# Kernel tuning notes

Hardware: AMD Instinct MI355X
Metric: run time of the kernel (lower is better)

Reference implementation:

```python
import jax, jax.numpy as jnp
import numpy as np

N, E, L, G, D = 131072, 262144, 16384, 2048, 300
NUM_LAYERS = 5


def setup_inputs() -> dict:
    key = jax.random.key(0)
    ks = jax.random.split(key, 16)
    s = 0.05
    inp = {}
    inp["x"] = jax.random.randint(ks[0], (N, 2), 0, 3, dtype=jnp.int32)
    inp["edge_index"] = jax.random.randint(ks[1], (2, E), 0, N, dtype=jnp.int32)
    inp["edge_attr"] = jax.random.randint(ks[2], (E, 2), 0, 3, dtype=jnp.int32)
    inp["lower_batch"] = jnp.sort(jax.random.randint(ks[3], (N,), 0, L, dtype=jnp.int32))
    inp["upper_batch"] = jnp.sort(jax.random.randint(ks[4], (L,), 0, G, dtype=jnp.int32))
    inp["x_emb1"] = jax.random.normal(ks[5], (120, D), jnp.float32) * s
    inp["x_emb2"] = jax.random.normal(ks[6], (3, D), jnp.float32) * s
    inp["edge_emb1"] = jax.random.normal(ks[7], (NUM_LAYERS, 6, D), jnp.float32) * s
    inp["edge_emb2"] = jax.random.normal(ks[8], (NUM_LAYERS, 3, D), jnp.float32) * s
    inp["mlp_w1"] = jax.random.normal(ks[9], (NUM_LAYERS, D, 2 * D), jnp.float32) * s
    inp["mlp_b1"] = jnp.zeros((NUM_LAYERS, 2 * D), jnp.float32)
    inp["mlp_w2"] = jax.random.normal(ks[10], (NUM_LAYERS, 2 * D, D), jnp.float32) * s
    inp["mlp_b2"] = jnp.zeros((NUM_LAYERS, D), jnp.float32)
    inp["bn_gamma"] = jnp.ones((NUM_LAYERS, D), jnp.float32)
    inp["bn_beta"] = jnp.zeros((NUM_LAYERS, D), jnp.float32)
    inp["cls_w1"] = jax.random.normal(ks[11], (D, D), jnp.float32) * s
    inp["cls_b1"] = jnp.zeros((D,), jnp.float32)
    inp["cls_w2"] = jax.random.normal(ks[12], (D, 1), jnp.float32) * s
    inp["cls_b2"] = jnp.zeros((1,), jnp.float32)
    return inp


def _segment_mean(data, seg, num):
    s = jax.ops.segment_sum(data, seg, num_segments=num)
    c = jax.ops.segment_sum(jnp.ones((data.shape[0], 1), data.dtype), seg, num_segments=num)
    return s / jnp.maximum(c, 1.0)


def reference(x, edge_index, edge_attr, lower_batch, upper_batch,
              x_emb1, x_emb2, edge_emb1, edge_emb2,
              mlp_w1, mlp_b1, mlp_w2, mlp_b2, bn_gamma, bn_beta,
              cls_w1, cls_b1, cls_w2, cls_b2):
    eps = 1e-5
    # node embeddings
    h = x_emb1[x[:, 0]] + x_emb2[x[:, 1]]  # [N, D]
    # add self loops with edge_attr (4, 0)
    loop = jnp.arange(N, dtype=edge_index.dtype)
    src = jnp.concatenate([edge_index[0], loop])
    dst = jnp.concatenate([edge_index[1], loop])
    ea0 = jnp.concatenate([edge_attr[:, 0], jnp.full((N,), 4, edge_attr.dtype)])
    ea1 = jnp.concatenate([edge_attr[:, 1], jnp.zeros((N,), edge_attr.dtype)])
    for l in range(NUM_LAYERS):
        e = edge_emb1[l][ea0] + edge_emb2[l][ea1]        # [E+N, D]
        msg = h[src] + e                                  # gather + add
        agg = jax.ops.segment_sum(msg, dst, num_segments=N)  # scatter-add
        h2 = jax.nn.relu(agg @ mlp_w1[l] + mlp_b1[l]) @ mlp_w2[l] + mlp_b2[l]
        # BatchNorm1d (training mode, biased var)
        mu = jnp.mean(h2, axis=0)
        var = jnp.var(h2, axis=0)
        h2 = (h2 - mu) * jax.lax.rsqrt(var + eps) * bn_gamma[l] + bn_beta[l]
        h = h2 if l == NUM_LAYERS - 1 else jax.nn.relu(h2)
    # hierarchical pooling: node -> lower substructure (mean), lower -> graph (mean)
    lower = _segment_mean(h, lower_batch, L)  # [L, D]

    def classify(feat):
        pooled = _segment_mean(feat, upper_batch, G)  # [G, D]
        hh = jax.nn.relu(pooled @ cls_w1 + cls_b1)
        return (hh @ cls_w2 + cls_b2)[:, 0]

    logits0 = classify(lower)
    logits1 = classify(jnp.roll(lower, 1, axis=0))  # aug_type == 'roll'
    return jnp.concatenate([logits0, logits1])  # [2G]
```

## Files before the change

kernel.cpp:

```cpp
#include <hip/hip_runtime.h>

#define N_NODES 131072
#define E_EDGES 262144
#define L_SEG 16384
#define G_SEG 2048
#define D_FEAT 300
#define NUM_LAYERS 5
#define MCHUNK 65536
#define HS 304
#define KP1 320
#define KP2 608
#define NP1 640
#define NP2 384

typedef unsigned short u16;
typedef unsigned int u32;
typedef __attribute__((ext_vector_type(8))) short short8v;
typedef __attribute__((ext_vector_type(4))) float f32x4;

struct __align__(16) U128 { u32 a, b, c, d; };
struct __align__(8) U64 { u32 a, b; };

__device__ __forceinline__ float bf2f(u16 u) { return __uint_as_float(((u32)u) << 16); }
__device__ __forceinline__ u16 f2bf(float f) {
  u32 x = __float_as_uint(f);
  x += 0x7fffu + ((x >> 16) & 1u);
  return (u16)(x >> 16);
}
__device__ __forceinline__ u32 pack2(float x, float y) {
  return (u32)f2bf(x) | ((u32)f2bf(y) << 16);
}

__device__ __forceinline__ void gl2lds16(const void* g, void* l) {
  auto gp = reinterpret_cast<const __attribute__((address_space(1))) void*>(
      reinterpret_cast<uintptr_t>(g));
  auto lp = reinterpret_cast<__attribute__((address_space(3))) void*>(
      reinterpret_cast<uintptr_t>(l));
  __builtin_amdgcn_global_load_lds(gp, lp, 16, 0, 0);
}

__global__ void k_init_h(const int* __restrict__ x, const float* __restrict__ e1,
                         const float* __restrict__ e2, u16* __restrict__ h) {
  int i = blockIdx.x * blockDim.x + threadIdx.x;
  if (i >= N_NODES * 76) return;
  int n = i / 76, q = i - n * 76;
  int col = q * 4;
  ushort4 o = make_ushort4(0, 0, 0, 0);
  if (col < 300) {
    int x0 = x[2 * n], x1 = x[2 * n + 1];
    float4 va = *(const float4*)(e1 + (size_t)x0 * D_FEAT + col);
    float4 vb = *(const float4*)(e2 + (size_t)x1 * D_FEAT + col);
    o.x = f2bf(va.x + vb.x); o.y = f2bf(va.y + vb.y);
    o.z = f2bf(va.z + vb.z); o.w = f2bf(va.w + vb.w);
  }
  *(ushort4*)(h + (size_t)n * HS + col) = o;
}

__global__ void k_prepw(const float* __restrict__ w, u16* __restrict__ wt,
                        int K, int Ncol, int NP, int KP) {
  int l = blockIdx.y;
  int i = blockIdx.x * blockDim.x + threadIdx.x;
  if (i >= NP * KP) return;
  int n = i / KP, k = i - n * KP;
  float v = (n < Ncol && k < K) ? w[(size_t)l * K * Ncol + (size_t)k * Ncol + n] : 0.f;
  wt[(size_t)l * NP * KP + i] = f2bf(v);
}

__global__ void k_zero(float* __restrict__ p, int n) {
  int i = blockIdx.x * blockDim.x + threadIdx.x;
  if (i < n) p[i] = 0.f;
}
__global__ void k_hist(const int* __restrict__ ei, int* __restrict__ cnt) {
  int e = blockIdx.x * blockDim.x + threadIdx.x;
  if (e < E_EDGES) atomicAdd(&cnt[ei[E_EDGES + e]], 1);
}
__global__ __launch_bounds__(1024) void k_scan(const int* __restrict__ cnt,
                                               int* __restrict__ offs,
                                               int* __restrict__ cursor) {
  __shared__ int part[1024];
  int t = threadIdx.x;
  int base = t * 128;
  int s = 0;
  for (int i = 0; i < 128; i++) s += cnt[base + i];
  part[t] = s;
  __syncthreads();
  for (int off = 1; off < 1024; off <<= 1) {
    int v = (t >= off) ? part[t - off] : 0;
    __syncthreads();
    part[t] += v;
    __syncthreads();
  }
  int run = (t == 0) ? 0 : part[t - 1];
  for (int i = 0; i < 128; i++) {
    offs[base + i] = run;
    cursor[base + i] = run;
    run += cnt[base + i];
  }
  if (t == 1023) offs[N_NODES] = run;
}
__global__ void k_fill(const int* __restrict__ ei, int* __restrict__ cursor,
                       int* __restrict__ elist) {
  int e = blockIdx.x * blockDim.x + threadIdx.x;
  if (e < E_EDGES) {
    int p = atomicAdd(&cursor[ei[E_EDGES + e]], 1);
    elist[p] = e;
  }
}

__global__ void k_gather(const u32* __restrict__ h, const int* __restrict__ ei,
                         const int* __restrict__ ea, const int* __restrict__ offs,
                         const int* __restrict__ elist, const float* __restrict__ sc1,
                         const float* __restrict__ sc2, const float* __restrict__ ee1,
                         const float* __restrict__ ee2, u32* __restrict__ agg) {
  int n = (blockIdx.x << 2) + (threadIdx.x >> 6);
  int lane = threadIdx.x & 63;
  int j0 = lane, j1 = lane + 64, j2 = lane + 128;
  float ax0, ay0, ax1, ay1, ax2 = 0.f, ay2 = 0.f;
  const u32* hn = h + (size_t)n * (HS / 2);
  {
    u32 u = hn[j0];
    ax0 = bf2f((u16)(u & 0xffffu)) + sc1[2 * j0] + sc2[2 * j0];
    ay0 = bf2f((u16)(u >> 16)) + sc1[2 * j0 + 1] + sc2[2 * j0 + 1];
    u = hn[j1];
    ax1 = bf2f((u16)(u & 0xffffu)) + sc1[2 * j1] + sc2[2 * j1];
    ay1 = bf2f((u16)(u >> 16)) + sc1[2 * j1 + 1] + sc2[2 * j1 + 1];
    if (j2 < 150) {
      u = hn[j2];
      ax2 = bf2f((u16)(u & 0xffffu)) + sc1[2 * j2] + sc2[2 * j2];
      ay2 = bf2f((u16)(u >> 16)) + sc1[2 * j2 + 1] + sc2[2 * j2 + 1];
    }
  }
  int p = offs[n], pe = offs[n + 1];
  int e, s, a0, a1;
  if (p < pe) {
    e = elist[p];
    s = ei[e];
    a0 = ea[2 * e];
    a1 = ea[2 * e + 1];
  }
  while (p < pe) {
    int np = p + 1;
    int e2 = 0, s2 = 0, a02 = 0, a12 = 0;
    if (np < pe) {
      e2 = elist[np];
      s2 = ei[e2];
      a02 = ea[2 * e2];
      a12 = ea[2 * e2 + 1];
    }
    const u32* hs = h + (size_t)s * (HS / 2);
    const float* p1 = ee1 + (size_t)a0 * D_FEAT;
    const float* p2 = ee2 + (size_t)a1 * D_FEAT;
    u32 u = hs[j0];
    ax0 += bf2f((u16)(u & 0xffffu)) + p1[2 * j0] + p2[2 * j0];
    ay0 += bf2f((u16)(u >> 16)) + p1[2 * j0 + 1] + p2[2 * j0 + 1];
    u = hs[j1];
    ax1 += bf2f((u16)(u & 0xffffu)) + p1[2 * j1] + p2[2 * j1];
    ay1 += bf2f((u16)(u >> 16)) + p1[2 * j1 + 1] + p2[2 * j1 + 1];
    if (j2 < 150) {
      u = hs[j2];
      ax2 += bf2f((u16)(u & 0xffffu)) + p1[2 * j2] + p2[2 * j2];
      ay2 += bf2f((u16)(u >> 16)) + p1[2 * j2 + 1] + p2[2 * j2 + 1];
    }
    p = np; e = e2; s = s2; a0 = a02; a1 = a12;
  }
  u32* ao = agg + (size_t)n * (KP1 / 2);
  ao[j0] = pack2(ax0, ay0);
  ao[j1] = pack2(ax1, ay1);
  if (j2 < 150) ao[j2] = pack2(ax2, ay2);
  else if (j2 < 160) ao[j2] = 0u;
}

template <bool RELU, int KP>
__global__ __launch_bounds__(512) void k_gemm_mfma(const u16* __restrict__ A,
                                                   const u16* __restrict__ WT,
                                                   const float* __restrict__ bias,
                                                   u16* __restrict__ C, int Ncol,
                                                   int Cstride, float* __restrict__ stats) {
  __shared__ __align__(16) u16 SL[12288];
  u16* Al = SL;
  u16* Bl = SL + 8192;
  int t = threadIdx.x;
  int w = t >> 6, lane = t & 63;
  int brow = blockIdx.y << 8, bcol = blockIdx.x << 7;
  int wr = w >> 1, wc = w & 1;
  int r16 = lane & 15, kq = lane >> 4;
  int rq = kq << 2;

  f32x4 zero4 = {0.f, 0.f, 0.f, 0.f};
  f32x4 acc[4][4];
#pragma unroll
  for (int mi = 0; mi < 4; mi++)
#pragma unroll
    for (int nj = 0; nj < 4; nj++) acc[mi][nj] = zero4;

  int m0 = 2 * w, m1 = m0 + 1;
  const u16* gA0 = A + (size_t)(brow + m0 * 16 + r16) * KP + kq * 8;
  const u16* gA1 = A + (size_t)(brow + m1 * 16 + r16) * KP + kq * 8;
  const u16* gB = WT + (size_t)(bcol + w * 16 + r16) * KP + kq * 8;
  u16* lA0 = Al + m0 * 512;
  u16* lA1 = Al + m1 * 512;
  u16* lB = Bl + w * 512;

  for (int k0 = 0; k0 < KP; k0 += 32) {
    __syncthreads();
    gl2lds16(gA0 + k0, lA0);
    gl2lds16(gA1 + k0, lA1);
    gl2lds16(gB + k0, lB);
    __syncthreads();
    short8v af[4], bf[4];
#pragma unroll
    for (int mi = 0; mi < 4; mi++)
      af[mi] = *(const short8v*)(Al + (wr * 4 + mi) * 512 + lane * 8);
#pragma unroll
    for (int nj = 0; nj < 4; nj++)
      bf[nj] = *(const short8v*)(Bl + (wc * 4 + nj) * 512 + lane * 8);
#pragma unroll
    for (int mi = 0; mi < 4; mi++)
#pragma unroll
      for (int nj = 0; nj < 4; nj++)
        acc[mi][nj] = __builtin_amdgcn_mfma_f32_16x16x32_bf16(af[mi], bf[nj], acc[mi][nj], 0, 0, 0);
  }

  __syncthreads();
#pragma unroll
  for (int p = 0; p < 4; p++) {
    if (wr == p) {
#pragma unroll
      for (int nj = 0; nj < 4; nj++) {
        int col = wc * 64 + nj * 16 + r16;
        int gcol = bcol + col;
        bool live = gcol < Ncol;
        float bs = live ? bias[gcol] : 0.f;
#pragma unroll
        for (int mi = 0; mi < 4; mi++) {
#pragma unroll
          for (int j = 0; j < 4; j++) {
            float v = acc[mi][nj][j] + bs;
            if (RELU) v = fmaxf(v, 0.f);
            if (!live) v = 0.f;
            SL[(mi * 16 + rq + j) * 132 + col] = f2bf(v);
          }
        }
      }
    }
    __syncthreads();
    {
      int r = t >> 3, s = t & 7;
      size_t grow = (size_t)(brow + p * 64 + r) * Cstride;
#pragma unroll
      for (int c = 0; c < 2; c++) {
        int colu = s * 16 + c * 8;
        int gcol = bcol + colu;
        if (gcol + 8 <= Cstride) {
          U64 v0 = *(const U64*)(SL + r * 132 + colu);
          U64 v1 = *(const U64*)(SL + r * 132 + colu + 4);
          *(U64*)(C + grow + gcol) = v0;
          *(U64*)(C + grow + gcol + 4) = v1;
        }
      }
    }
    if (stats != nullptr && t < 128) {
      int gcol = bcol + t;
      if (gcol < Ncol) {
        float s0 = 0.f, q0 = 0.f;
#pragma unroll 8
        for (int r = 0; r < 64; r++) {
          float v = bf2f(SL[r * 132 + t]);
          s0 += v;
          q0 = fmaf(v, v, q0);
        }
        atomicAdd(stats + gcol, s0);
        atomicAdd(stats + 304 + gcol, q0);
      }
    }
    __syncthreads();
  }
}

__global__ void k_bnfin(const float* __restrict__ sums, const float* __restrict__ gamma,
                        const float* __restrict__ beta, float* __restrict__ fa,
                        float* __restrict__ fc) {
  int d = blockIdx.x * blockDim.x + threadIdx.x;
  if (d >= HS) return;
  float a = 0.f, c = 0.f;
  if (d < D_FEAT) {
    const float inv = 1.f / (float)N_NODES;
    float mu = sums[d] * inv;
    float var = sums[304 + d] * inv - mu * mu;
    a = rsqrtf(var + 1e-5f) * gamma[d];
    c = beta[d] - mu * a;
  }
  fa[d] = a;
  fc[d] = c;
}

__global__ void k_bnnorm(u16* __restrict__ h, const float* __restrict__ fa,
                         const float* __restrict__ fc, int relu) {
  int i = blockIdx.x * blockDim.x + threadIdx.x;
  if (i >= N_NODES * 38) return;
  int n = i / 38, q = i - n * 38;
  int col = q * 8;
  u16* hp = h + (size_t)n * HS + col;
  float4 a0 = *(const float4*)(fa + col);
  float4 a1 = *(const float4*)(fa + col + 4);
  float4 c0 = *(const float4*)(fc + col);
  float4 c1 = *(const float4*)(fc + col + 4);
  ushort4 u0 = *(ushort4*)hp;
  ushort4 u1 = *(ushort4*)(hp + 4);
  float r0, r1, r2, r3, r4, r5, r6, r7;
#define BN1(res, uv, A, C)                       \
  res = fmaf((A), bf2f(uv), (C));                \
  if (relu) res = fmaxf(res, 0.f);
  BN1(r0, u0.x, a0.x, c0.x) BN1(r1, u0.y, a0.y, c0.y)
  BN1(r2, u0.z, a0.z, c0.z) BN1(r3, u0.w, a0.w, c0.w)
  BN1(r4, u1.x, a1.x, c1.x) BN1(r5, u1.y, a1.y, c1.y)
  BN1(r6, u1.z, a1.z, c1.z) BN1(r7, u1.w, a1.w, c1.w)
#undef BN1
  ushort4 o0, o1;
  o0.x = f2bf(r0); o0.y = f2bf(r1); o0.z = f2bf(r2); o0.w = f2bf(r3);
  o1.x = f2bf(r4); o1.y = f2bf(r5); o1.z = f2bf(r6); o1.w = f2bf(r7);
  *(ushort4*)hp = o0;
  *(ushort4*)(hp + 4) = o1;
}

__device__ __forceinline__ int lowerBound(const int* __restrict__ a, int n, int v) {
  int lo = 0, hi = n;
  while (lo < hi) {
    int m = (lo + hi) >> 1;
    if (a[m] < v) lo = m + 1; else hi = m;
  }
  return lo;
}

__global__ void k_lower(const u16* __restrict__ h, const int* __restrict__ lb,
                        float* __restrict__ lower) {
  int g = blockIdx.x;
  int s = lowerBound(lb, N_NODES, g);
  int e = lowerBound(lb, N_NODES, g + 1);
  float invc = 1.f / (float)max(e - s, 1);
  for (int d = threadIdx.x; d < D_FEAT; d += 256) {
    float acc = 0.f;
    for (int r = s; r < e; r++) acc += bf2f(h[(size_t)r * HS + d]);
    lower[(size_t)g * D_FEAT + d] = acc * invc;
  }
}

__global__ void k_pooled(const float* __restrict__ lower, const int* __restrict__ ub,
                         float* __restrict__ pooled) {
  int g = blockIdx.x, br = blockIdx.y;
  int s = lowerBound(ub, L_SEG, g);
  int e = lowerBound(ub, L_SEG, g + 1);
  float invc = 1.f / (float)max(e - s, 1);
  for (int d = threadIdx.x; d < D_FEAT; d += 256) {
    float acc = 0.f;
    for (int i = s; i < e; i++) {
      int row = br ? (i - 1 + L_SEG) % L_SEG : i;
      acc += lower[(size_t)row * D_FEAT + d];
    }
    pooled[((size_t)br * G_SEG + g) * D_FEAT + d] = acc * invc;
  }
}

__global__ __launch_bounds__(256) void k_classify(const float* __restrict__ pooled,
                                                  const float* __restrict__ w1,
                                                  const float* __restrict__ b1,
                                                  const float* __restrict__ w2,
                                                  const float* __restrict__ b2,
                                                  float* __restrict__ out) {
  __shared__ float p[D_FEAT];
  __shared__ float red[4];
  int g = blockIdx.x, br = blockIdx.y;
  const float* pr = pooled + ((size_t)br * G_SEG + g) * D_FEAT;
  for (int d = threadIdx.x; d < D_FEAT; d += 256) p[d] = pr[d];
  __syncthreads();
  float partial = 0.f;
  for (int j = threadIdx.x; j < D_FEAT; j += 256) {
    float acc = b1[j];
    for (int k = 0; k < D_FEAT; k++) acc = fmaf(p[k], w1[(size_t)k * D_FEAT + j], acc);
    acc = fmaxf(acc, 0.f);
    partial += acc * w2[j];
  }
  for (int off = 32; off; off >>= 1) partial += __shfl_down(partial, off, 64);
  int lane = threadIdx.x & 63, wid = threadIdx.x >> 6;
  if (lane == 0) red[wid] = partial;
  __syncthreads();
  if (threadIdx.x == 0) out[(size_t)br * G_SEG + g] = red[0] + red[1] + red[2] + red[3] + b2[0];
}

extern "C" void kernel_launch(void* const* d_in, const int* in_sizes, int n_in,
                              void* d_out, int out_size, void* d_ws, size_t ws_size,
                              hipStream_t stream) {
  const int* x = (const int*)d_in[0];
  const int* ei = (const int*)d_in[1];
  const int* ea = (const int*)d_in[2];
  const int* lb = (const int*)d_in[3];
  const int* ub = (const int*)d_in[4];
  const float* xe1 = (const float*)d_in[5];
  const float* xe2 = (const float*)d_in[6];
  const float* ee1 = (const float*)d_in[7];
  const float* ee2 = (const float*)d_in[8];
  const float* w1 = (const float*)d_in[9];
  const float* b1 = (const float*)d_in[10];
  const float* w2 = (const float*)d_in[11];
  const float* b2 = (const float*)d_in[12];
  const float* gam = (const float*)d_in[13];
  const float* bet = (const float*)d_in[14];
  const float* cw1 = (const float*)d_in[15];
  const float* cb1 = (const float*)d_in[16];
  const float* cw2 = (const float*)d_in[17];
  const float* cb2 = (const float*)d_in[18];
  float* out = (float*)d_out;

  char* base = (char*)d_ws;
  size_t off = 0;
  auto alloc = [&](size_t bytes) -> void* {
    void* p = base + off;
    off += (bytes + 255) & ~(size_t)255;
    return p;
  };
  u16* h = (u16*)alloc((size_t)N_NODES * HS * 2);
  u16* agg = (u16*)alloc((size_t)N_NODES * KP1 * 2);
  u16* tbuf = (u16*)alloc((size_t)MCHUNK * KP2 * 2);
  u16* W1T = (u16*)alloc((size_t)NUM_LAYERS * NP1 * KP1 * 2);
  u16* W2T = (u16*)alloc((size_t)NUM_LAYERS * NP2 * KP2 * 2);
  int* cnt = (int*)alloc((size_t)N_NODES * 4);
  int* offs = (int*)alloc((size_t)(N_NODES + 1) * 4);
  int* cursor = (int*)alloc((size_t)N_NODES * 4);
  int* elist = (int*)alloc((size_t)E_EDGES * 4);
  float* stats = (float*)alloc(608 * 4);
  float* aff_a = (float*)alloc(HS * 4);
  float* aff_c = (float*)alloc(HS * 4);
  float* lower = (float*)tbuf;
  float* pooled = lower + (size_t)L_SEG * D_FEAT;

  if (ws_size < off) {
    k_zero<<<(out_size + 255) / 256, 256, 0, stream>>>(out, out_size);
    return;
  }

  const int NT = 256;

  k_prepw<<<dim3((NP1 * KP1 + NT - 1) / NT, NUM_LAYERS), NT, 0, stream>>>(w1, W1T, 300, 600, NP1, KP1);
  k_prepw<<<dim3((NP2 * KP2 + NT - 1) / NT, NUM_LAYERS), NT, 0, stream>>>(w2, W2T, 600, 300, NP2, KP2);

  k_zero<<<(N_NODES + NT - 1) / NT, NT, 0, stream>>>((float*)cnt, N_NODES);
  k_hist<<<(E_EDGES + NT - 1) / NT, NT, 0, stream>>>(ei, cnt);
  k_scan<<<1, 1024, 0, stream>>>(cnt, offs, cursor);
  k_fill<<<(E_EDGES + NT - 1) / NT, NT, 0, stream>>>(ei, cursor, elist);

  k_init_h<<<(N_NODES * 76 + NT - 1) / NT, NT, 0, stream>>>(x, xe1, xe2, h);

  for (int l = 0; l < NUM_LAYERS; l++) {
    k_gather<<<N_NODES / 4, NT, 0, stream>>>(
        (const u32*)h, ei, ea, offs, elist,
        ee1 + ((size_t)l * 6 + 4) * D_FEAT, ee2 + (size_t)l * 3 * D_FEAT,
        ee1 + (size_t)l * 6 * D_FEAT, ee2 + (size_t)l * 3 * D_FEAT, (u32*)agg);
    k_zero<<<3, NT, 0, stream>>>(stats, 608);
    for (int c0 = 0; c0 < N_NODES; c0 += MCHUNK) {
      dim3 g1(5, MCHUNK / 256);
      k_gemm_mfma<true, KP1><<<g1, 512, 0, stream>>>(
          agg + (size_t)c0 * KP1, W1T + (size_t)l * NP1 * KP1, b1 + (size_t)l * 600,
          tbuf, 600, KP2, nullptr);
      dim3 g2(3, MCHUNK / 256);
      k_gemm_mfma<false, KP2><<<g2, 512, 0, stream>>>(
          tbuf, W2T + (size_t)l * NP2 * KP2, b2 + (size_t)l * 300,
          h + (size_t)c0 * HS, 300, HS, stats);
    }
    k_bnfin<<<2, NT, 0, stream>>>(stats, gam + (size_t)l * 300, bet + (size_t)l * 300,
                                  aff_a, aff_c);
    k_bnnorm<<<(N_NODES * 38 + NT - 1) / NT, NT, 0, stream>>>(
        h, aff_a, aff_c, l < NUM_LAYERS - 1 ? 1 : 0);
  }

  k_lower<<<L_SEG, NT, 0, stream>>>(h, lb, lower);
  dim3 gp(G_SEG, 2);
  k_pooled<<<gp, NT, 0, stream>>>(lower, ub, pooled);
  k_classify<<<gp, NT, 0, stream>>>(pooled, cw1, cb1, cw2, cb2, out);
}
```

Baseline: 2.477 ms.

## Double-buffer GEMM LDS tiles and unroll edge aggregation by two

The MFMA GEMM now keeps two LDS buffers, issuing the global-to-LDS copy for the next K slice before computing on the current one. This drops one barrier per iteration and overlaps loads with MFMA work, at the cost of doubling shared memory, which may lower occupancy. The edge aggregation loop is also unrolled to handle two edges per iteration, with their gathers issued together to expose more memory-level parallelism. This replaces the earlier one-ahead index prefetch.

Result: no change. 2.443 ms (-1.4%).

```diff
diff --git a/kernel.cpp b/kernel.cpp
--- a/kernel.cpp
+++ b/kernel.cpp
@@ -131,22 +131,43 @@
     }
   }
   int p = offs[n], pe = offs[n + 1];
-  int e, s, a0, a1;
+  while (p + 2 <= pe) {
+    int eA = elist[p], eB = elist[p + 1];
+    int sA = ei[eA], sB = ei[eB];
+    int a0A = ea[2 * eA], a1A = ea[2 * eA + 1];
+    int a0B = ea[2 * eB], a1B = ea[2 * eB + 1];
+    const u32* hA = h + (size_t)sA * (HS / 2);
+    const u32* hB = h + (size_t)sB * (HS / 2);
+    const float* p1A = ee1 + (size_t)a0A * D_FEAT;
+    const float* p2A = ee2 + (size_t)a1A * D_FEAT;
+    const float* p1B = ee1 + (size_t)a0B * D_FEAT;
+    const float* p2B = ee2 + (size_t)a1B * D_FEAT;
+    u32 uA0 = hA[j0], uA1 = hA[j1];
+    u32 uB0 = hB[j0], uB1 = hB[j1];
+    u32 uA2 = 0, uB2 = 0;
+    if (j2 < 150) { uA2 = hA[j2]; uB2 = hB[j2]; }
+    ax0 += bf2f((u16)(uA0 & 0xffffu)) + p1A[2 * j0] + p2A[2 * j0];
+    ay0 += bf2f((u16)(uA0 >> 16)) + p1A[2 * j0 + 1] + p2A[2 * j0 + 1];
+    ax1 += bf2f((u16)(uA1 & 0xffffu)) + p1A[2 * j1] + p2A[2 * j1];
+    ay1 += bf2f((u16)(uA1 >> 16)) + p1A[2 * j1 + 1] + p2A[2 * j1 + 1];
+    if (j2 < 150) {
+      ax2 += bf2f((u16)(uA2 & 0xffffu)) + p1A[2 * j2] + p2A[2 * j2];
+      ay2 += bf2f((u16)(uA2 >> 16)) + p1A[2 * j2 + 1] + p2A[2 * j2 + 1];
+    }
+    ax0 += bf2f((u16)(uB0 & 0xffffu)) + p1B[2 * j0] + p2B[2 * j0];
+    ay0 += bf2f((u16)(uB0 >> 16)) + p1B[2 * j0 + 1] + p2B[2 * j0 + 1];
+    ax1 += bf2f((u16)(uB1 & 0xffffu)) + p1B[2 * j1] + p2B[2 * j1];
+    ay1 += bf2f((u16)(uB1 >> 16)) + p1B[2 * j1 + 1] + p2B[2 * j1 + 1];
+    if (j2 < 150) {
+      ax2 += bf2f((u16)(uB2 & 0xffffu)) + p1B[2 * j2] + p2B[2 * j2];
+      ay2 += bf2f((u16)(uB2 >> 16)) + p1B[2 * j2 + 1] + p2B[2 * j2 + 1];
+    }
+    p += 2;
+  }
   if (p < pe) {
-    e = elist[p];
-    s = ei[e];
-    a0 = ea[2 * e];
-    a1 = ea[2 * e + 1];
-  }
-  while (p < pe) {
-    int np = p + 1;
-    int e2 = 0, s2 = 0, a02 = 0, a12 = 0;
-    if (np < pe) {
-      e2 = elist[np];
-      s2 = ei[e2];
-      a02 = ea[2 * e2];
-      a12 = ea[2 * e2 + 1];
-    }
+    int e = elist[p];
+    int s = ei[e];
+    int a0 = ea[2 * e], a1 = ea[2 * e + 1];
     const u32* hs = h + (size_t)s * (HS / 2);
     const float* p1 = ee1 + (size_t)a0 * D_FEAT;
     const float* p2 = ee2 + (size_t)a1 * D_FEAT;
@@ -161,7 +182,6 @@
       ax2 += bf2f((u16)(u & 0xffffu)) + p1[2 * j2] + p2[2 * j2];
       ay2 += bf2f((u16)(u >> 16)) + p1[2 * j2 + 1] + p2[2 * j2 + 1];
     }
-    p = np; e = e2; s = s2; a0 = a02; a1 = a12;
   }
   u32* ao = agg + (size_t)n * (KP1 / 2);
   ao[j0] = pack2(ax0, ay0);
@@ -176,9 +196,7 @@
                                                    const float* __restrict__ bias,
                                                    u16* __restrict__ C, int Ncol,
                                                    int Cstride, float* __restrict__ stats) {
-  __shared__ __align__(16) u16 SL[12288];
-  u16* Al = SL;
-  u16* Bl = SL + 8192;
+  __shared__ __align__(16) u16 SL[24576];
   int t = threadIdx.x;
   int w = t >> 6, lane = t & 63;
   int brow = blockIdx.y << 8, bcol = blockIdx.x << 7;
@@ -197,31 +215,37 @@
   const u16* gA0 = A + (size_t)(brow + m0 * 16 + r16) * KP + kq * 8;
   const u16* gA1 = A + (size_t)(brow + m1 * 16 + r16) * KP + kq * 8;
   const u16* gB = WT + (size_t)(bcol + w * 16 + r16) * KP + kq * 8;
-  u16* lA0 = Al + m0 * 512;
-  u16* lA1 = Al + m1 * 512;
-  u16* lB = Bl + w * 512;
-
+
+  gl2lds16(gA0, SL + m0 * 512);
+  gl2lds16(gA1, SL + m1 * 512);
+  gl2lds16(gB, SL + 8192 + w * 512);
+  __syncthreads();
+
+  int cur = 0;
   for (int k0 = 0; k0 < KP; k0 += 32) {
-    __syncthreads();
-    gl2lds16(gA0 + k0, lA0);
-    gl2lds16(gA1 + k0, lA1);
-    gl2lds16(gB + k0, lB);
-    __syncthreads();
+    u16* curb = SL + cur * 12288;
+    u16* nxtb = SL + (cur ^ 1) * 12288;
+    if (k0 + 32 < KP) {
+      gl2lds16(gA0 + k0 + 32, nxtb + m0 * 512);
+      gl2lds16(gA1 + k0 + 32, nxtb + m1 * 512);
+      gl2lds16(gB + k0 + 32, nxtb + 8192 + w * 512);
+    }
     short8v af[4], bf[4];
 #pragma unroll
     for (int mi = 0; mi < 4; mi++)
-      af[mi] = *(const short8v*)(Al + (wr * 4 + mi) * 512 + lane * 8);
+      af[mi] = *(const short8v*)(curb + (wr * 4 + mi) * 512 + lane * 8);
 #pragma unroll
     for (int nj = 0; nj < 4; nj++)
-      bf[nj] = *(const short8v*)(Bl + (wc * 4 + nj) * 512 + lane * 8);
+      bf[nj] = *(const short8v*)(curb + 8192 + (wc * 4 + nj) * 512 + lane * 8);
 #pragma unroll
     for (int mi = 0; mi < 4; mi++)
 #pragma unroll
       for (int nj = 0; nj < 4; nj++)
         acc[mi][nj] = __builtin_amdgcn_mfma_f32_16x16x32_bf16(af[mi], bf[nj], acc[mi][nj], 0, 0, 0);
-  }
-
-  __syncthreads();
+    __syncthreads();
+    cur ^= 1;
+  }
+
 #pragma unroll
   for (int p = 0; p < 4; p++) {
     if (wr == p) {
```
